# Kernel tuning notes

Measured on AMD Instinct MI355X. Metric: run time of the kernel, lower is better.

Reference implementation:

```python
import jax, jax.numpy as jnp
import numpy as np

B, N, D, R, H, E = 4, 8192, 16, 32, 64, 262144


def _linear_init(key, fan_in, fan_out):
    return jax.random.normal(key, (fan_in, fan_out), jnp.float32) * (1.0 / np.sqrt(fan_in))


def setup_inputs() -> dict:
    key = jax.random.key(0)
    ks = jax.random.split(key, 8)
    particles = jax.random.normal(ks[0], (B, N, D), jnp.float32)
    senders = jax.random.randint(ks[1], (E,), 0, N, dtype=jnp.int32)
    receivers = jax.random.randint(ks[2], (E,), 0, N, dtype=jnp.int32)
    # relation_encoder: Linear(2D->H), ReLU, Linear(H->R), ReLU
    W1 = _linear_init(ks[3], 2 * D, H)
    b1 = jnp.zeros((H,), jnp.float32)
    W2 = _linear_init(ks[4], H, R)
    b2 = jnp.zeros((R,), jnp.float32)
    # dynamics_fn: Linear(D+R->H), ReLU, Linear(H->D)
    W3 = _linear_init(ks[5], D + R, H)
    b3 = jnp.zeros((H,), jnp.float32)
    W4 = _linear_init(ks[6], H, D)
    b4 = jnp.zeros((D,), jnp.float32)
    return {"particles": particles, "senders": senders, "receivers": receivers,
            "W1": W1, "b1": b1, "W2": W2, "b2": b2,
            "W3": W3, "b3": b3, "W4": W4, "b4": b4}


def reference(particles, senders, receivers, W1, b1, W2, b2, W3, b3, W4, b4):
    # Gather per-edge sender/receiver states: [B, E, D]
    send = particles[:, senders, :]
    recv = particles[:, receivers, :]
    edge_in = jnp.concatenate([send, recv], axis=-1)          # [B, E, 2D]
    # relation_encoder (one batched GEMM over all edges)
    h = jax.nn.relu(edge_in @ W1 + b1)                        # [B, E, H]
    rel_feat = jax.nn.relu(h @ W2 + b2)                       # [B, E, R]
    # scatter-add edge features into receiver nodes
    Bp, Np, _ = particles.shape
    rel = jnp.zeros((Bp, Np, rel_feat.shape[-1]), particles.dtype)
    rel = rel.at[:, receivers, :].add(rel_feat)               # [B, N, R]
    # node update MLP
    dyn_in = jnp.concatenate([particles, rel], axis=-1)       # [B, N, D+R]
    delta = jax.nn.relu(dyn_in @ W3 + b3) @ W4 + b4           # [B, N, D]
    return particles + delta
```

## Files before the change

### kernel.cpp

```cpp
#include <hip/hip_runtime.h>
#include <hip/hip_bf16.h>

namespace {

constexpr int B = 4;
constexpr int N = 8192;
constexpr int D = 16;
constexpr int R = 32;
constexpr int H = 64;
constexpr int E = 262144;

typedef __attribute__((ext_vector_type(8))) short short8;
typedef __attribute__((ext_vector_type(4))) short short4v;
typedef __attribute__((ext_vector_type(4))) float f32x4;

__device__ __forceinline__ float4 ld4(const float* p) {
    return *reinterpret_cast<const float4*>(p);
}
__device__ __forceinline__ float4 fma4(float a, float4 w, float4 c) {
    return float4{fmaf(a, w.x, c.x), fmaf(a, w.y, c.y),
                  fmaf(a, w.z, c.z), fmaf(a, w.w, c.w)};
}
__device__ __forceinline__ float4 relu4(float4 v) {
    return float4{fmaxf(v.x, 0.f), fmaxf(v.y, 0.f), fmaxf(v.z, 0.f), fmaxf(v.w, 0.f)};
}
__device__ __forceinline__ short bf16s(float f) {
    __hip_bfloat16 h = __float2bfloat16(f);
    return __builtin_bit_cast(short, h);
}
__device__ __forceinline__ short8 pack8(float4 a, float4 b) {
    short8 o;
    o[0] = bf16s(a.x); o[1] = bf16s(a.y); o[2] = bf16s(a.z); o[3] = bf16s(a.w);
    o[4] = bf16s(b.x); o[5] = bf16s(b.y); o[6] = bf16s(b.z); o[7] = bf16s(b.w);
    return o;
}
__device__ __forceinline__ short4v pack4_relu(f32x4 c) {
    short4v o;
    o[0] = bf16s(fmaxf(c[0], 0.f)); o[1] = bf16s(fmaxf(c[1], 0.f));
    o[2] = bf16s(fmaxf(c[2], 0.f)); o[3] = bf16s(fmaxf(c[3], 0.f));
    return o;
}

constexpr int RED_S = 260;

__global__ __launch_bounds__(256) void hist_prepack_kernel(
    const int* __restrict__ receivers, int* __restrict__ cnt,
    const float* __restrict__ W1, const float* __restrict__ W2,
    const float* __restrict__ W3, const float* __restrict__ W4,
    short* __restrict__ w1p, short* __restrict__ w2p,
    short* __restrict__ w3p, short* __restrict__ w4p,
    float4* __restrict__ relz)
{
    if (blockIdx.x < 1024) {
        int e = blockIdx.x * 256 + threadIdx.x;
        atomicAdd(cnt + receivers[e], 1);
        return;
    }
    if (blockIdx.x >= 1025) {
        const int base = (blockIdx.x - 1025) * 256 + threadIdx.x;
        #pragma unroll
        for (int i = 0; i < 8; ++i)
            relz[base + i * 32768] = float4{0.f, 0.f, 0.f, 0.f};
        return;
    }
    const int t = threadIdx.x;
    for (int i = t; i < 4 * 64 * 8; i += 256) {
        int j = i & 7, lane = (i >> 3) & 63, ct = i >> 9;
        int k = (lane >> 4) * 8 + j, n = ct * 16 + (lane & 15);
        w1p[i] = bf16s(W1[k * H + n]);
    }
    for (int i = t; i < 4 * 64 * 8; i += 256) {
        int j = i & 7, lane = (i >> 3) & 63, idx = i >> 9;
        int ct = idx >> 1, kc = idx & 1;
        int k = kc * 32 + (lane >> 4) * 8 + j, f = ct * 16 + (lane & 15);
        w2p[i] = bf16s(W2[k * R + f]);
    }
    for (int i = t; i < 8 * 64 * 8; i += 256) {
        int j = i & 7, lane = (i >> 3) & 63, idx = i >> 9;
        int ct = idx >> 1, kc = idx & 1;
        int k = kc * 32 + (lane >> 4) * 8 + j, n = ct * 16 + (lane & 15);
        w3p[i] = (k < D + R) ? bf16s(W3[k * H + n]) : (short)0;
    }
    for (int i = t; i < 2 * 64 * 8; i += 256) {
        int j = i & 7, lane = (i >> 3) & 63, kc = i >> 9;
        int k = kc * 32 + (lane >> 4) * 8 + j, d = lane & 15;
        w4p[i] = bf16s(W4[k * D + d]);
    }
}

__global__ __launch_bounds__(1024) void scan_kernel(
    const int* __restrict__ cnt, int* __restrict__ pos)
{
    __shared__ int wtot[16];
    const int t = threadIdx.x;
    const int lane = t & 63;
    int local[8];
    int s = 0;
    #pragma unroll
    for (int i = 0; i < 8; ++i) { local[i] = cnt[t * 8 + i]; s += local[i]; }
    int incl = s;
    #pragma unroll
    for (int d = 1; d < 64; d <<= 1) {
        int v = __shfl_up(incl, d, 64);
        if (lane >= d) incl += v;
    }
    if (lane == 63) wtot[t >> 6] = incl;
    __syncthreads();
    int base = incl - s;
    const int wv = t >> 6;
    #pragma unroll
    for (int i = 0; i < 16; ++i) base += (i < wv) ? wtot[i] : 0;
    #pragma unroll
    for (int i = 0; i < 8; ++i) {
        pos[t * 8 + i] = base;
        base += local[i];
    }
}

__global__ __launch_bounds__(256) void scatter_kernel(
    const int* __restrict__ senders, const int* __restrict__ receivers,
    int* __restrict__ pos, int2* __restrict__ sr)
{
    int e = blockIdx.x * 256 + threadIdx.x;
    if (e < E) {
        int r = receivers[e];
        int p = atomicAdd(pos + r, 1);
        sr[p] = int2{senders[e], r};
    }
}

__global__ __launch_bounds__(256, 3) void edge_mfma_kernel(
    const float* __restrict__ particles,
    const int2*  __restrict__ sr,
    const short* __restrict__ w1p, const float* __restrict__ b1,
    const short* __restrict__ w2p, const float* __restrict__ b2,
    float* __restrict__ rel)
{
    __shared__ float red[31 * RED_S + 256];
    __shared__ short hbuf[4][16 * 72];
    __shared__ int   rs[256];

    const int tid  = threadIdx.x;
    const int lane = tid & 63;
    const int w    = tid >> 6;
    const int b    = blockIdx.x >> 10;
    const int p0   = (blockIdx.x & 1023) * 256;
    const int l15  = lane & 15;
    const int q    = lane >> 4;

    const int2 srv = sr[p0 + tid];
    const int sval = srv.x;
    const int rval = srv.y;
    rs[tid] = rval;

    float4 a0[4], a1[4];
    #pragma unroll
    for (int t = 0; t < 4; ++t) {
        int srow = __shfl(sval, t * 16 + l15);
        int rrow = __shfl(rval, t * 16 + l15);
        int row = (q < 2) ? srow : rrow;
        const float* src = particles + ((size_t)b * N + row) * D + (q & 1) * 8;
        a0[t] = ld4(src);
        a1[t] = ld4(src + 4);
    }

    short8 w1f[4], w2f[4];
    #pragma unroll
    for (int mt = 0; mt < 4; ++mt)
        w1f[mt] = *reinterpret_cast<const short8*>(w1p + (mt * 64 + lane) * 8);
    #pragma unroll
    for (int i = 0; i < 4; ++i)
        w2f[i] = *reinterpret_cast<const short8*>(w2p + (i * 64 + lane) * 8);

    f32x4 bias1[4];
    #pragma unroll
    for (int mt = 0; mt < 4; ++mt) {
        float4 t4 = ld4(b1 + mt * 16 + q * 4);
        bias1[mt] = f32x4{t4.x, t4.y, t4.z, t4.w};
    }
    const float bias2a = b2[l15];
    const float bias2b = b2[16 + l15];

    short8 af[4];
    #pragma unroll
    for (int t = 0; t < 4; ++t) af[t] = pack8(a0[t], a1[t]);

    short* hb = &hbuf[w][0];

    #pragma unroll
    for (int t = 0; t < 4; ++t) {
        #pragma unroll
        for (int mt = 0; mt < 4; ++mt) {
            f32x4 c = bias1[mt];
            c = __builtin_amdgcn_mfma_f32_16x16x32_bf16(w1f[mt], af[t], c, 0, 0, 0);
            *reinterpret_cast<short4v*>(hb + l15 * 72 + mt * 16 + q * 4) = pack4_relu(c);
        }
        short8 h0 = *reinterpret_cast<const short8*>(hb + l15 * 72 + q * 8);
        short8 h1 = *reinterpret_cast<const short8*>(hb + l15 * 72 + 32 + q * 8);

        f32x4 r0 = {bias2a, bias2a, bias2a, bias2a};
        f32x4 r1 = {bias2b, bias2b, bias2b, bias2b};
        r0 = __builtin_amdgcn_mfma_f32_16x16x32_bf16(h0, w2f[0], r0, 0, 0, 0);
        r0 = __builtin_amdgcn_mfma_f32_16x16x32_bf16(h1, w2f[1], r0, 0, 0, 0);
        r1 = __builtin_amdgcn_mfma_f32_16x16x32_bf16(h0, w2f[2], r1, 0, 0, 0);
        r1 = __builtin_amdgcn_mfma_f32_16x16x32_bf16(h1, w2f[3], r1, 0, 0, 0);

        const int pb = w * 64 + t * 16 + q * 4;
        *reinterpret_cast<f32x4*>(red + l15 * RED_S + pb) =
            f32x4{fmaxf(r0[0], 0.f), fmaxf(r0[1], 0.f), fmaxf(r0[2], 0.f), fmaxf(r0[3], 0.f)};
        *reinterpret_cast<f32x4*>(red + (16 + l15) * RED_S + pb) =
            f32x4{fmaxf(r1[0], 0.f), fmaxf(r1[1], 0.f), fmaxf(r1[2], 0.f), fmaxf(r1[3], 0.f)};
    }
    __syncthreads();

    const int g = tid >> 5;
    const int f = tid & 31;
    const int base = g * 32;

    f32x4 v4[8];
    #pragma unroll
    for (int i = 0; i < 8; ++i)
        v4[i] = *reinterpret_cast<const f32x4*>(red + f * RED_S + base + 4 * i);
    int4 r4[8];
    #pragma unroll
    for (int i = 0; i < 8; ++i)
        r4[i] = *reinterpret_cast<const int4*>(rs + base + 4 * i);

    const int first = r4[0].x;
    const int last  = r4[7].w;
    if (first == last) {
        float acc = 0.f;
        #pragma unroll
        for (int i = 0; i < 8; ++i)
            acc += (v4[i][0] + v4[i][1]) + (v4[i][2] + v4[i][3]);
        atomicAdd(rel + ((size_t)b * N + first) * R + f, acc);
    } else {
        float acc = 0.f;
        int cur = first;
        #pragma unroll
        for (int i = 0; i < 32; ++i) {
            int rr = (i & 3) == 0 ? r4[i >> 2].x : (i & 3) == 1 ? r4[i >> 2].y
                   : (i & 3) == 2 ? r4[i >> 2].z : r4[i >> 2].w;
            float v = v4[i >> 2][i & 3];
            if (rr != cur) {
                atomicAdd(rel + ((size_t)b * N + cur) * R + f, acc);
                acc = 0.f;
                cur = rr;
            }
            acc += v;
        }
        atomicAdd(rel + ((size_t)b * N + cur) * R + f, acc);
    }
}

__global__ __launch_bounds__(256, 4) void node_mfma_kernel(
    const float* __restrict__ particles,
    const float* __restrict__ rel,
    const short* __restrict__ w3p, const float* __restrict__ b3,
    const short* __restrict__ w4p, const float* __restrict__ b4,
    float* __restrict__ out)
{
    __shared__ short hbuf[4][16 * 72];

    const int tid  = threadIdx.x;
    const int lane = tid & 63;
    const int w    = tid >> 6;
    const int tile = blockIdx.x * 4 + w;
    const int b    = tile >> 9;
    const int l15  = lane & 15;
    const int q    = lane >> 4;
    const int node = (tile & 511) * 16 + l15;

    const float* prow = particles + ((size_t)b * N + node) * D;
    const float* rrow = rel + ((size_t)b * N + node) * R;

    const float* src0 = (q < 2) ? (prow + (q & 1) * 8) : (rrow + (q & 1) * 8);
    float4 c0a = ld4(src0), c0b = ld4(src0 + 4);
    float4 c1a = {0.f, 0.f, 0.f, 0.f}, c1b = {0.f, 0.f, 0.f, 0.f};
    if (q < 2) { c1a = ld4(rrow + 16 + q * 8); c1b = ld4(rrow + 20 + q * 8); }

    short8 w3f[8], w4f[2];
    #pragma unroll
    for (int i = 0; i < 8; ++i)
        w3f[i] = *reinterpret_cast<const short8*>(w3p + (i * 64 + lane) * 8);
    #pragma unroll
    for (int i = 0; i < 2; ++i)
        w4f[i] = *reinterpret_cast<const short8*>(w4p + (i * 64 + lane) * 8);

    f32x4 bias3[4];
    #pragma unroll
    for (int mt = 0; mt < 4; ++mt) {
        float4 t4 = ld4(b3 + mt * 16 + q * 4);
        bias3[mt] = f32x4{t4.x, t4.y, t4.z, t4.w};
    }
    f32x4 bias4;
    { float4 t4 = ld4(b4 + q * 4); bias4 = f32x4{t4.x, t4.y, t4.z, t4.w}; }

    short8 a0 = pack8(c0a, c0b);
    short8 a1 = pack8(c1a, c1b);

    short* hb = &hbuf[w][0];
    #pragma unroll
    for (int mt = 0; mt < 4; ++mt) {
        f32x4 c = bias3[mt];
        c = __builtin_amdgcn_mfma_f32_16x16x32_bf16(w3f[mt * 2 + 0], a0, c, 0, 0, 0);
        c = __builtin_amdgcn_mfma_f32_16x16x32_bf16(w3f[mt * 2 + 1], a1, c, 0, 0, 0);
        *reinterpret_cast<short4v*>(hb + l15 * 72 + mt * 16 + q * 4) = pack4_relu(c);
    }
    short8 h0 = *reinterpret_cast<const short8*>(hb + l15 * 72 + q * 8);
    short8 h1 = *reinterpret_cast<const short8*>(hb + l15 * 72 + 32 + q * 8);

    f32x4 r = bias4;
    r = __builtin_amdgcn_mfma_f32_16x16x32_bf16(w4f[0], h0, r, 0, 0, 0);
    r = __builtin_amdgcn_mfma_f32_16x16x32_bf16(w4f[1], h1, r, 0, 0, 0);

    float4 pv = ld4(prow + q * 4);
    float4* po = reinterpret_cast<float4*>(out + ((size_t)b * N + node) * D + q * 4);
    *po = float4{pv.x + r[0], pv.y + r[1], pv.z + r[2], pv.w + r[3]};
}


__global__ __launch_bounds__(256, 2) void edge_atomic_kernel(
    const float* __restrict__ particles,
    const int*   __restrict__ senders,
    const int*   __restrict__ receivers,
    const float* __restrict__ W1, const float* __restrict__ b1,
    const float* __restrict__ W2, const float* __restrict__ b2,
    float* __restrict__ rel)
{
    const int idx = blockIdx.x * 256 + threadIdx.x;
    const int b = idx >> 18;
    const int e = idx & (E - 1);
    const int s = senders[e];
    const int r = receivers[e];

    float4 ein4[8];
    {
        const float4* ps = reinterpret_cast<const float4*>(particles + ((size_t)b * N + s) * D);
        const float4* pr = reinterpret_cast<const float4*>(particles + ((size_t)b * N + r) * D);
        #pragma unroll
        for (int qq = 0; qq < 4; ++qq) ein4[qq] = ps[qq];
        #pragma unroll
        for (int qq = 0; qq < 4; ++qq) ein4[4 + qq] = pr[qq];
    }
    float4 rf4[8];
    #pragma unroll
    for (int qq = 0; qq < 8; ++qq) rf4[qq] = ld4(b2 + 4 * qq);

    for (int j4 = 0; j4 < H / 4; ++j4) {
        float4 h = ld4(b1 + 4 * j4);
        const float* w1c = W1 + 4 * j4;
        #pragma unroll
        for (int kv = 0; kv < 8; ++kv) {
            const float4 ev = ein4[kv];
            h = fma4(ev.x, ld4(w1c + (4 * kv + 0) * H), h);
            h = fma4(ev.y, ld4(w1c + (4 * kv + 1) * H), h);
            h = fma4(ev.z, ld4(w1c + (4 * kv + 2) * H), h);
            h = fma4(ev.w, ld4(w1c + (4 * kv + 3) * H), h);
        }
        h = relu4(h);
        const float* w2r = W2 + (4 * j4) * R;
        #pragma unroll
        for (int qq = 0; qq < 4; ++qq) {
            const float hq = (qq == 0) ? h.x : (qq == 1) ? h.y : (qq == 2) ? h.z : h.w;
            #pragma unroll
            for (int r4 = 0; r4 < 8; ++r4)
                rf4[r4] = fma4(hq, ld4(w2r + qq * R + 4 * r4), rf4[r4]);
        }
    }
    float* dst = rel + ((size_t)b * N + r) * R;
    #pragma unroll
    for (int r4 = 0; r4 < 8; ++r4) {
        float4 v = relu4(rf4[r4]);
        atomicAdd(dst + 4 * r4 + 0, v.x);
        atomicAdd(dst + 4 * r4 + 1, v.y);
        atomicAdd(dst + 4 * r4 + 2, v.z);
        atomicAdd(dst + 4 * r4 + 3, v.w);
    }
}

__global__ __launch_bounds__(256, 2) void node_valu_kernel(
    const float* __restrict__ particles,
    const float* __restrict__ rel,
    const float* __restrict__ W3, const float* __restrict__ b3,
    const float* __restrict__ W4, const float* __restrict__ b4,
    float* __restrict__ out)
{
    const int idx = blockIdx.x * 256 + threadIdx.x;
    float4 in4[12];
    {
        const float4* pp = reinterpret_cast<const float4*>(particles + (size_t)idx * D);
        #pragma unroll
        for (int qq = 0; qq < 4; ++qq) in4[qq] = pp[qq];
        const float4* pr = reinterpret_cast<const float4*>(rel + (size_t)idx * R);
        #pragma unroll
        for (int qq = 0; qq < 8; ++qq) in4[4 + qq] = pr[qq];
    }
    float4 dl4[4];
    #pragma unroll
    for (int qq = 0; qq < 4; ++qq) dl4[qq] = ld4(b4 + 4 * qq);

    for (int j4 = 0; j4 < H / 4; ++j4) {
        float4 h = ld4(b3 + 4 * j4);
        const float* w3c = W3 + 4 * j4;
        #pragma unroll
        for (int kv = 0; kv < 12; ++kv) {
            const float4 ev = in4[kv];
            h = fma4(ev.x, ld4(w3c + (4 * kv + 0) * H), h);
            h = fma4(ev.y, ld4(w3c + (4 * kv + 1) * H), h);
            h = fma4(ev.z, ld4(w3c + (4 * kv + 2) * H), h);
            h = fma4(ev.w, ld4(w3c + (4 * kv + 3) * H), h);
        }
        h = relu4(h);
        const float* w4r = W4 + (4 * j4) * D;
        #pragma unroll
        for (int qq = 0; qq < 4; ++qq) {
            const float hq = (qq == 0) ? h.x : (qq == 1) ? h.y : (qq == 2) ? h.z : h.w;
            #pragma unroll
            for (int d4 = 0; d4 < 4; ++d4)
                dl4[d4] = fma4(hq, ld4(w4r + qq * D + 4 * d4), dl4[d4]);
        }
    }
    float4* po = reinterpret_cast<float4*>(out + (size_t)idx * D);
    #pragma unroll
    for (int qq = 0; qq < 4; ++qq) {
        float4 v = dl4[qq];
        float4 pv = in4[qq];
        po[qq] = float4{pv.x + v.x, pv.y + v.y, pv.z + v.z, pv.w + v.w};
    }
}

}

extern "C" void kernel_launch(void* const* d_in, const int* in_sizes, int n_in,
                              void* d_out, int out_size, void* d_ws, size_t ws_size,
                              hipStream_t stream) {
    const float* particles = (const float*)d_in[0];
    const int*   senders   = (const int*)d_in[1];
    const int*   receivers = (const int*)d_in[2];
    const float* W1 = (const float*)d_in[3];
    const float* b1 = (const float*)d_in[4];
    const float* W2 = (const float*)d_in[5];
    const float* b2 = (const float*)d_in[6];
    const float* W3 = (const float*)d_in[7];
    const float* b3 = (const float*)d_in[8];
    const float* W4 = (const float*)d_in[9];
    const float* b4 = (const float*)d_in[10];
    float* out = (float*)d_out;

    char* ws = (char*)d_ws;
    size_t off = 0;
    auto take = [&](size_t bytes) -> char* {
        char* p = ws + off;
        off = (off + bytes + 255) & ~(size_t)255;
        return p;
    };
    int*   cnt     = (int*)  take((size_t)N * 4);
    int*   pos     = (int*)  take((size_t)N * 4);
    int2*  sr      = (int2*) take((size_t)E * 8);
    float* rel     = (float*)take((size_t)B * N * R * 4);
    short* w1p     = (short*)take((size_t)4 * 64 * 8 * 2);
    short* w2p     = (short*)take((size_t)4 * 64 * 8 * 2);
    short* w3p     = (short*)take((size_t)8 * 64 * 8 * 2);
    short* w4p     = (short*)take((size_t)2 * 64 * 8 * 2);
    const bool fast = (off <= ws_size);

    if (fast) {
        hipMemsetAsync(cnt, 0, (size_t)N * 4, stream);
        hist_prepack_kernel<<<1025 + 128, 256, 0, stream>>>(
            receivers, cnt, W1, W2, W3, W4, w1p, w2p, w3p, w4p, (float4*)rel);
        scan_kernel<<<1, 1024, 0, stream>>>(cnt, pos);
        scatter_kernel<<<E / 256, 256, 0, stream>>>(senders, receivers, pos, sr);
        edge_mfma_kernel<<<(B * E) / 256, 256, 0, stream>>>(
            particles, sr, w1p, b1, w2p, b2, rel);
        node_mfma_kernel<<<(B * N / 16) / 4, 256, 0, stream>>>(
            particles, rel, w3p, b3, w4p, b4, out);
    } else {
        float* rel0 = (float*)d_ws;
        hipMemsetAsync(rel0, 0, (size_t)B * N * R * 4, stream);
        edge_atomic_kernel<<<(B * E) / 256, 256, 0, stream>>>(
            particles, senders, receivers, W1, b1, W2, b2, rel0);
        node_valu_kernel<<<(B * N) / 256, 256, 0, stream>>>(
            particles, rel0, W3, b3, W4, b4, out);
    }
}
```

Measured before the change: 140.0 us.

## Fuse sort preprocessing into one cooperative kernel and shrink edge reduction buffer to bf16

Replaces the memset, histogram/prepack, scan and scatter launches with a single cooperative kernel that uses grid-wide syncs between phases. This removes several kernel launch gaps and the separate memset. The edge kernel also stores its per-edge relation features as bf16 in shared memory instead of fp32, which halves LDS use and allows a higher occupancy hint (4 blocks per CU). The cost is lower precision in the scatter-add inputs, plus a single 1024-thread scan run by one 256-thread block. It falls back to the old path if the cooperative launch fails.

```diff
diff --git a/kernel.cpp b/kernel.cpp
--- a/kernel.cpp
+++ b/kernel.cpp
@@ -1,5 +1,8 @@
 #include <hip/hip_runtime.h>
 #include <hip/hip_bf16.h>
+#include <hip/hip_cooperative_groups.h>
+
+namespace cg = cooperative_groups;
 
 namespace {
 
@@ -40,8 +43,121 @@
     o[2] = bf16s(fmaxf(c[2], 0.f)); o[3] = bf16s(fmaxf(c[3], 0.f));
     return o;
 }
-
-constexpr int RED_S = 260;
+__device__ __forceinline__ float red_get(const int4* uu, int i) {
+    const int wsel = i >> 1;
+    const int4 v = uu[wsel >> 2];
+    const int word = (wsel & 3) == 0 ? v.x : (wsel & 3) == 1 ? v.y
+                   : (wsel & 3) == 2 ? v.z : v.w;
+    return (i & 1) ? __builtin_bit_cast(float, word & 0xffff0000)
+                   : __builtin_bit_cast(float, (unsigned)word << 16);
+}
+
+constexpr int RED_S = 264;
+
+__device__ __forceinline__ void prepack_w12(
+    int t, const float* __restrict__ W1, const float* __restrict__ W2,
+    short* __restrict__ w1p, short* __restrict__ w2p)
+{
+    for (int i = t; i < 4 * 64 * 8; i += 256) {
+        int j = i & 7, lane = (i >> 3) & 63, ct = i >> 9;
+        int k = (lane >> 4) * 8 + j, n = ct * 16 + (lane & 15);
+        w1p[i] = bf16s(W1[k * H + n]);
+    }
+    for (int i = t; i < 4 * 64 * 8; i += 256) {
+        int j = i & 7, lane = (i >> 3) & 63, idx = i >> 9;
+        int ct = idx >> 1, kc = idx & 1;
+        int k = kc * 32 + (lane >> 4) * 8 + j, f = ct * 16 + (lane & 15);
+        w2p[i] = bf16s(W2[k * R + f]);
+    }
+}
+__device__ __forceinline__ void prepack_w34(
+    int t, const float* __restrict__ W3, const float* __restrict__ W4,
+    short* __restrict__ w3p, short* __restrict__ w4p)
+{
+    for (int i = t; i < 8 * 64 * 8; i += 256) {
+        int j = i & 7, lane = (i >> 3) & 63, idx = i >> 9;
+        int ct = idx >> 1, kc = idx & 1;
+        int k = kc * 32 + (lane >> 4) * 8 + j, n = ct * 16 + (lane & 15);
+        w3p[i] = (k < D + R) ? bf16s(W3[k * H + n]) : (short)0;
+    }
+    for (int i = t; i < 2 * 64 * 8; i += 256) {
+        int j = i & 7, lane = (i >> 3) & 63, kc = i >> 9;
+        int k = kc * 32 + (lane >> 4) * 8 + j, d = lane & 15;
+        w4p[i] = bf16s(W4[k * D + d]);
+    }
+}
+
+__global__ __launch_bounds__(256) void sort_coop_kernel(
+    const int* __restrict__ senders, const int* __restrict__ receivers,
+    const float* __restrict__ W1, const float* __restrict__ W2,
+    const float* __restrict__ W3, const float* __restrict__ W4,
+    int* __restrict__ cnt, int* __restrict__ pos, int2* __restrict__ sr,
+    short* __restrict__ w1p, short* __restrict__ w2p,
+    short* __restrict__ w3p, short* __restrict__ w4p,
+    float4* __restrict__ relz)
+{
+    cg::grid_group grid = cg::this_grid();
+    const int t = threadIdx.x;
+    const int blk = blockIdx.x;
+
+    if (blk < 128) {
+        const int base = blk * 256 + t;
+        #pragma unroll
+        for (int i = 0; i < 8; ++i)
+            relz[base + i * 32768] = float4{0.f, 0.f, 0.f, 0.f};
+    } else if (blk < 160) {
+        cnt[(blk - 128) * 256 + t] = 0;
+    } else if (blk == 160) {
+        prepack_w12(t, W1, W2, w1p, w2p);
+    } else if (blk == 161) {
+        prepack_w34(t, W3, W4, w3p, w4p);
+    }
+    grid.sync();
+
+    {
+        const int base = blk * 1024 + t;
+        #pragma unroll
+        for (int i = 0; i < 4; ++i)
+            atomicAdd(cnt + receivers[base + i * 256], 1);
+    }
+    grid.sync();
+
+    if (blk == 0) {
+        __shared__ int wtot[4];
+        int local[32];
+        int s = 0;
+        #pragma unroll
+        for (int i = 0; i < 32; ++i) { local[i] = cnt[t * 32 + i]; s += local[i]; }
+        int incl = s;
+        const int lane = t & 63;
+        #pragma unroll
+        for (int d = 1; d < 64; d <<= 1) {
+            int v = __shfl_up(incl, d, 64);
+            if (lane >= d) incl += v;
+        }
+        if (lane == 63) wtot[t >> 6] = incl;
+        __syncthreads();
+        int base = incl - s;
+        const int wv = t >> 6;
+        #pragma unroll
+        for (int i = 0; i < 4; ++i) base += (i < wv) ? wtot[i] : 0;
+        #pragma unroll
+        for (int i = 0; i < 32; ++i) { pos[t * 32 + i] = base; base += local[i]; }
+    }
+    grid.sync();
+
+    {
+        const int base = blk * 1024 + t;
+        #pragma unroll
+        for (int i = 0; i < 4; ++i) {
+            const int e = base + i * 256;
+            const int r = receivers[e];
+            const int p = atomicAdd(pos + r, 1);
+            sr[p] = int2{senders[e], r};
+        }
+    }
+}
+
 
 __global__ __launch_bounds__(256) void hist_prepack_kernel(
     const int* __restrict__ receivers, int* __restrict__ cnt,
@@ -63,29 +179,8 @@
             relz[base + i * 32768] = float4{0.f, 0.f, 0.f, 0.f};
         return;
     }
-    const int t = threadIdx.x;
-    for (int i = t; i < 4 * 64 * 8; i += 256) {
-        int j = i & 7, lane = (i >> 3) & 63, ct = i >> 9;
-        int k = (lane >> 4) * 8 + j, n = ct * 16 + (lane & 15);
-        w1p[i] = bf16s(W1[k * H + n]);
-    }
-    for (int i = t; i < 4 * 64 * 8; i += 256) {
-        int j = i & 7, lane = (i >> 3) & 63, idx = i >> 9;
-        int ct = idx >> 1, kc = idx & 1;
-        int k = kc * 32 + (lane >> 4) * 8 + j, f = ct * 16 + (lane & 15);
-        w2p[i] = bf16s(W2[k * R + f]);
-    }
-    for (int i = t; i < 8 * 64 * 8; i += 256) {
-        int j = i & 7, lane = (i >> 3) & 63, idx = i >> 9;
-        int ct = idx >> 1, kc = idx & 1;
-        int k = kc * 32 + (lane >> 4) * 8 + j, n = ct * 16 + (lane & 15);
-        w3p[i] = (k < D + R) ? bf16s(W3[k * H + n]) : (short)0;
-    }
-    for (int i = t; i < 2 * 64 * 8; i += 256) {
-        int j = i & 7, lane = (i >> 3) & 63, kc = i >> 9;
-        int k = kc * 32 + (lane >> 4) * 8 + j, d = lane & 15;
-        w4p[i] = bf16s(W4[k * D + d]);
-    }
+    prepack_w12(threadIdx.x, W1, W2, w1p, w2p);
+    prepack_w34(threadIdx.x, W3, W4, w3p, w4p);
 }
 
 __global__ __launch_bounds__(1024) void scan_kernel(
@@ -129,14 +224,14 @@
     }
 }
 
-__global__ __launch_bounds__(256, 3) void edge_mfma_kernel(
+__global__ __launch_bounds__(256, 4) void edge_mfma_kernel(
     const float* __restrict__ particles,
     const int2*  __restrict__ sr,
     const short* __restrict__ w1p, const float* __restrict__ b1,
     const short* __restrict__ w2p, const float* __restrict__ b2,
     float* __restrict__ rel)
 {
-    __shared__ float red[31 * RED_S + 256];
+    __shared__ short red[R * RED_S];
     __shared__ short hbuf[4][16 * 72];
     __shared__ int   rs[256];
 
@@ -206,10 +301,8 @@
         r1 = __builtin_amdgcn_mfma_f32_16x16x32_bf16(h1, w2f[3], r1, 0, 0, 0);
 
         const int pb = w * 64 + t * 16 + q * 4;
-        *reinterpret_cast<f32x4*>(red + l15 * RED_S + pb) =
-            f32x4{fmaxf(r0[0], 0.f), fmaxf(r0[1], 0.f), fmaxf(r0[2], 0.f), fmaxf(r0[3], 0.f)};
-        *reinterpret_cast<f32x4*>(red + (16 + l15) * RED_S + pb) =
-            f32x4{fmaxf(r1[0], 0.f), fmaxf(r1[1], 0.f), fmaxf(r1[2], 0.f), fmaxf(r1[3], 0.f)};
+        *reinterpret_cast<short4v*>(red + l15 * RED_S + pb)        = pack4_relu(r0);
+        *reinterpret_cast<short4v*>(red + (16 + l15) * RED_S + pb) = pack4_relu(r1);
     }
     __syncthreads();
 
@@ -217,10 +310,10 @@
     const int f = tid & 31;
     const int base = g * 32;
 
-    f32x4 v4[8];
-    #pragma unroll
-    for (int i = 0; i < 8; ++i)
-        v4[i] = *reinterpret_cast<const f32x4*>(red + f * RED_S + base + 4 * i);
+    int4 uu[4];
+    #pragma unroll
+    for (int i = 0; i < 4; ++i)
+        uu[i] = *reinterpret_cast<const int4*>(red + f * RED_S + base + 8 * i);
     int4 r4[8];
     #pragma unroll
     for (int i = 0; i < 8; ++i)
@@ -231,8 +324,7 @@
     if (first == last) {
         float acc = 0.f;
         #pragma unroll
-        for (int i = 0; i < 8; ++i)
-            acc += (v4[i][0] + v4[i][1]) + (v4[i][2] + v4[i][3]);
+        for (int i = 0; i < 32; ++i) acc += red_get(uu, i);
         atomicAdd(rel + ((size_t)b * N + first) * R + f, acc);
     } else {
         float acc = 0.f;
@@ -241,7 +333,7 @@
         for (int i = 0; i < 32; ++i) {
             int rr = (i & 3) == 0 ? r4[i >> 2].x : (i & 3) == 1 ? r4[i >> 2].y
                    : (i & 3) == 2 ? r4[i >> 2].z : r4[i >> 2].w;
-            float v = v4[i >> 2][i & 3];
+            float v = red_get(uu, i);
             if (rr != cur) {
                 atomicAdd(rel + ((size_t)b * N + cur) * R + f, acc);
                 acc = 0.f;
@@ -466,11 +558,23 @@
     const bool fast = (off <= ws_size);
 
     if (fast) {
-        hipMemsetAsync(cnt, 0, (size_t)N * 4, stream);
-        hist_prepack_kernel<<<1025 + 128, 256, 0, stream>>>(
-            receivers, cnt, W1, W2, W3, W4, w1p, w2p, w3p, w4p, (float4*)rel);
-        scan_kernel<<<1, 1024, 0, stream>>>(cnt, pos);
-        scatter_kernel<<<E / 256, 256, 0, stream>>>(senders, receivers, pos, sr);
+        float4* relz = (float4*)rel;
+        void* cargs[] = {
+            (void*)&senders, (void*)&receivers,
+            (void*)&W1, (void*)&W2, (void*)&W3, (void*)&W4,
+            (void*)&cnt, (void*)&pos, (void*)&sr,
+            (void*)&w1p, (void*)&w2p, (void*)&w3p, (void*)&w4p,
+            (void*)&relz
+        };
+        hipError_t ce = hipLaunchCooperativeKernel(
+            (const void*)sort_coop_kernel, dim3(256), dim3(256), cargs, 0, stream);
+        if (ce != hipSuccess) {
+            hipMemsetAsync(cnt, 0, (size_t)N * 4, stream);
+            hist_prepack_kernel<<<1153, 256, 0, stream>>>(
+                receivers, cnt, W1, W2, W3, W4, w1p, w2p, w3p, w4p, relz);
+            scan_kernel<<<1, 1024, 0, stream>>>(cnt, pos);
+            scatter_kernel<<<E / 256, 256, 0, stream>>>(senders, receivers, pos, sr);
+        }
         edge_mfma_kernel<<<(B * E) / 256, 256, 0, stream>>>(
             particles, sr, w1p, b1, w2p, b2, rel);
         node_mfma_kernel<<<(B * N / 16) / 4, 256, 0, stream>>>(
```

Measured after the change: 236.2 us. 68.8% more time.

## Loop batches inside edge kernel, prefetch next batch gathers, store reduction in bf16

Applied to the files above, without the earlier changes.

The edge kernel now processes all four batches per block, so the sender/receiver index loads and row offsets are reused across batches. The particle gathers for the next batch are issued before the current batch's MFMA work to hide their latency. The shared-memory reduction buffer switches from fp32 to bf16 to halve its LDS footprint. In exchange there are four times fewer blocks, an extra barrier per batch, and the relation features lose precision before the scatter-add.

```diff
diff --git a/kernel.cpp b/kernel.cpp
--- a/kernel.cpp
+++ b/kernel.cpp
@@ -40,8 +40,50 @@
     o[2] = bf16s(fmaxf(c[2], 0.f)); o[3] = bf16s(fmaxf(c[3], 0.f));
     return o;
 }
-
-constexpr int RED_S = 260;
+__device__ __forceinline__ float red_get(const int4* uu, int i) {
+    const int wsel = i >> 1;
+    const int4 v = uu[wsel >> 2];
+    const int word = (wsel & 3) == 0 ? v.x : (wsel & 3) == 1 ? v.y
+                   : (wsel & 3) == 2 ? v.z : v.w;
+    return (i & 1) ? __builtin_bit_cast(float, word & 0xffff0000)
+                   : __builtin_bit_cast(float, (unsigned)word << 16);
+}
+
+constexpr int RED_S = 264;
+
+__device__ __forceinline__ void prepack_w12(
+    int t, const float* __restrict__ W1, const float* __restrict__ W2,
+    short* __restrict__ w1p, short* __restrict__ w2p)
+{
+    for (int i = t; i < 4 * 64 * 8; i += 256) {
+        int j = i & 7, lane = (i >> 3) & 63, ct = i >> 9;
+        int k = (lane >> 4) * 8 + j, n = ct * 16 + (lane & 15);
+        w1p[i] = bf16s(W1[k * H + n]);
+    }
+    for (int i = t; i < 4 * 64 * 8; i += 256) {
+        int j = i & 7, lane = (i >> 3) & 63, idx = i >> 9;
+        int ct = idx >> 1, kc = idx & 1;
+        int k = kc * 32 + (lane >> 4) * 8 + j, f = ct * 16 + (lane & 15);
+        w2p[i] = bf16s(W2[k * R + f]);
+    }
+}
+__device__ __forceinline__ void prepack_w34(
+    int t, const float* __restrict__ W3, const float* __restrict__ W4,
+    short* __restrict__ w3p, short* __restrict__ w4p)
+{
+    for (int i = t; i < 8 * 64 * 8; i += 256) {
+        int j = i & 7, lane = (i >> 3) & 63, idx = i >> 9;
+        int ct = idx >> 1, kc = idx & 1;
+        int k = kc * 32 + (lane >> 4) * 8 + j, n = ct * 16 + (lane & 15);
+        w3p[i] = (k < D + R) ? bf16s(W3[k * H + n]) : (short)0;
+    }
+    for (int i = t; i < 2 * 64 * 8; i += 256) {
+        int j = i & 7, lane = (i >> 3) & 63, kc = i >> 9;
+        int k = kc * 32 + (lane >> 4) * 8 + j, d = lane & 15;
+        w4p[i] = bf16s(W4[k * D + d]);
+    }
+}
+
 
 __global__ __launch_bounds__(256) void hist_prepack_kernel(
     const int* __restrict__ receivers, int* __restrict__ cnt,
@@ -63,29 +105,8 @@
             relz[base + i * 32768] = float4{0.f, 0.f, 0.f, 0.f};
         return;
     }
-    const int t = threadIdx.x;
-    for (int i = t; i < 4 * 64 * 8; i += 256) {
-        int j = i & 7, lane = (i >> 3) & 63, ct = i >> 9;
-        int k = (lane >> 4) * 8 + j, n = ct * 16 + (lane & 15);
-        w1p[i] = bf16s(W1[k * H + n]);
-    }
-    for (int i = t; i < 4 * 64 * 8; i += 256) {
-        int j = i & 7, lane = (i >> 3) & 63, idx = i >> 9;
-        int ct = idx >> 1, kc = idx & 1;
-        int k = kc * 32 + (lane >> 4) * 8 + j, f = ct * 16 + (lane & 15);
-        w2p[i] = bf16s(W2[k * R + f]);
-    }
-    for (int i = t; i < 8 * 64 * 8; i += 256) {
-        int j = i & 7, lane = (i >> 3) & 63, idx = i >> 9;
-        int ct = idx >> 1, kc = idx & 1;
-        int k = kc * 32 + (lane >> 4) * 8 + j, n = ct * 16 + (lane & 15);
-        w3p[i] = (k < D + R) ? bf16s(W3[k * H + n]) : (short)0;
-    }
-    for (int i = t; i < 2 * 64 * 8; i += 256) {
-        int j = i & 7, lane = (i >> 3) & 63, kc = i >> 9;
-        int k = kc * 32 + (lane >> 4) * 8 + j, d = lane & 15;
-        w4p[i] = bf16s(W4[k * D + d]);
-    }
+    prepack_w12(threadIdx.x, W1, W2, w1p, w2p);
+    prepack_w34(threadIdx.x, W3, W4, w3p, w4p);
 }
 
 __global__ __launch_bounds__(1024) void scan_kernel(
@@ -136,32 +157,26 @@
     const short* __restrict__ w2p, const float* __restrict__ b2,
     float* __restrict__ rel)
 {
-    __shared__ float red[31 * RED_S + 256];
+    __shared__ short red[R * RED_S];
     __shared__ short hbuf[4][16 * 72];
     __shared__ int   rs[256];
 
     const int tid  = threadIdx.x;
     const int lane = tid & 63;
     const int w    = tid >> 6;
-    const int b    = blockIdx.x >> 10;
-    const int p0   = (blockIdx.x & 1023) * 256;
+    const int p0   = blockIdx.x * 256;
     const int l15  = lane & 15;
     const int q    = lane >> 4;
 
     const int2 srv = sr[p0 + tid];
-    const int sval = srv.x;
-    const int rval = srv.y;
-    rs[tid] = rval;
-
-    float4 a0[4], a1[4];
+    rs[tid] = srv.y;
+
+    int rowoff[4];
     #pragma unroll
     for (int t = 0; t < 4; ++t) {
-        int srow = __shfl(sval, t * 16 + l15);
-        int rrow = __shfl(rval, t * 16 + l15);
-        int row = (q < 2) ? srow : rrow;
-        const float* src = particles + ((size_t)b * N + row) * D + (q & 1) * 8;
-        a0[t] = ld4(src);
-        a1[t] = ld4(src + 4);
+        int srow = __shfl(srv.x, t * 16 + l15);
+        int rrow = __shfl(srv.y, t * 16 + l15);
+        rowoff[t] = ((q < 2) ? srow : rrow) * D + (q & 1) * 8;
     }
 
     short8 w1f[4], w2f[4];
@@ -181,75 +196,96 @@
     const float bias2a = b2[l15];
     const float bias2b = b2[16 + l15];
 
-    short8 af[4];
-    #pragma unroll
-    for (int t = 0; t < 4; ++t) af[t] = pack8(a0[t], a1[t]);
+    float4 ga[4], gb[4];
+    #pragma unroll
+    for (int t = 0; t < 4; ++t) {
+        const float* src = particles + rowoff[t];
+        ga[t] = ld4(src);
+        gb[t] = ld4(src + 4);
+    }
 
     short* hb = &hbuf[w][0];
 
-    #pragma unroll
-    for (int t = 0; t < 4; ++t) {
-        #pragma unroll
-        for (int mt = 0; mt < 4; ++mt) {
-            f32x4 c = bias1[mt];
-            c = __builtin_amdgcn_mfma_f32_16x16x32_bf16(w1f[mt], af[t], c, 0, 0, 0);
-            *reinterpret_cast<short4v*>(hb + l15 * 72 + mt * 16 + q * 4) = pack4_relu(c);
-        }
-        short8 h0 = *reinterpret_cast<const short8*>(hb + l15 * 72 + q * 8);
-        short8 h1 = *reinterpret_cast<const short8*>(hb + l15 * 72 + 32 + q * 8);
-
-        f32x4 r0 = {bias2a, bias2a, bias2a, bias2a};
-        f32x4 r1 = {bias2b, bias2b, bias2b, bias2b};
-        r0 = __builtin_amdgcn_mfma_f32_16x16x32_bf16(h0, w2f[0], r0, 0, 0, 0);
-        r0 = __builtin_amdgcn_mfma_f32_16x16x32_bf16(h1, w2f[1], r0, 0, 0, 0);
-        r1 = __builtin_amdgcn_mfma_f32_16x16x32_bf16(h0, w2f[2], r1, 0, 0, 0);
-        r1 = __builtin_amdgcn_mfma_f32_16x16x32_bf16(h1, w2f[3], r1, 0, 0, 0);
-
-        const int pb = w * 64 + t * 16 + q * 4;
-        *reinterpret_cast<f32x4*>(red + l15 * RED_S + pb) =
-            f32x4{fmaxf(r0[0], 0.f), fmaxf(r0[1], 0.f), fmaxf(r0[2], 0.f), fmaxf(r0[3], 0.f)};
-        *reinterpret_cast<f32x4*>(red + (16 + l15) * RED_S + pb) =
-            f32x4{fmaxf(r1[0], 0.f), fmaxf(r1[1], 0.f), fmaxf(r1[2], 0.f), fmaxf(r1[3], 0.f)};
-    }
-    __syncthreads();
-
-    const int g = tid >> 5;
-    const int f = tid & 31;
-    const int base = g * 32;
-
-    f32x4 v4[8];
-    #pragma unroll
-    for (int i = 0; i < 8; ++i)
-        v4[i] = *reinterpret_cast<const f32x4*>(red + f * RED_S + base + 4 * i);
-    int4 r4[8];
-    #pragma unroll
-    for (int i = 0; i < 8; ++i)
-        r4[i] = *reinterpret_cast<const int4*>(rs + base + 4 * i);
-
-    const int first = r4[0].x;
-    const int last  = r4[7].w;
-    if (first == last) {
-        float acc = 0.f;
-        #pragma unroll
-        for (int i = 0; i < 8; ++i)
-            acc += (v4[i][0] + v4[i][1]) + (v4[i][2] + v4[i][3]);
-        atomicAdd(rel + ((size_t)b * N + first) * R + f, acc);
-    } else {
-        float acc = 0.f;
-        int cur = first;
-        #pragma unroll
-        for (int i = 0; i < 32; ++i) {
-            int rr = (i & 3) == 0 ? r4[i >> 2].x : (i & 3) == 1 ? r4[i >> 2].y
-                   : (i & 3) == 2 ? r4[i >> 2].z : r4[i >> 2].w;
-            float v = v4[i >> 2][i & 3];
-            if (rr != cur) {
-                atomicAdd(rel + ((size_t)b * N + cur) * R + f, acc);
-                acc = 0.f;
-                cur = rr;
+    for (int bb = 0; bb < B; ++bb) {
+        short8 af[4];
+        #pragma unroll
+        for (int t = 0; t < 4; ++t) af[t] = pack8(ga[t], gb[t]);
+
+        if (bb + 1 < B) {
+            const float* pb = particles + (size_t)(bb + 1) * N * D;
+            #pragma unroll
+            for (int t = 0; t < 4; ++t) {
+                const float* src = pb + rowoff[t];
+                ga[t] = ld4(src);
+                gb[t] = ld4(src + 4);
             }
-            acc += v;
-        }
-        atomicAdd(rel + ((size_t)b * N + cur) * R + f, acc);
+        }
+
+        #pragma unroll
+        for (int t = 0; t < 4; ++t) {
+            #pragma unroll
+            for (int mt = 0; mt < 4; ++mt) {
+                f32x4 c = bias1[mt];
+                c = __builtin_amdgcn_mfma_f32_16x16x32_bf16(w1f[mt], af[t], c, 0, 0, 0);
+                *reinterpret_cast<short4v*>(hb + l15 * 72 + mt * 16 + q * 4) = pack4_relu(c);
+            }
+            short8 h0 = *reinterpret_cast<const short8*>(hb + l15 * 72 + q * 8);
+            short8 h1 = *reinterpret_cast<const short8*>(hb + l15 * 72 + 32 + q * 8);
+
+            f32x4 r0 = {bias2a, bias2a, bias2a, bias2a};
+            f32x4 r1 = {bias2b, bias2b, bias2b, bias2b};
+            r0 = __builtin_amdgcn_mfma_f32_16x16x32_bf16(h0, w2f[0], r0, 0, 0, 0);
+            r0 = __builtin_amdgcn_mfma_f32_16x16x32_bf16(h1, w2f[1], r0, 0, 0, 0);
+            r1 = __builtin_amdgcn_mfma_f32_16x16x32_bf16(h0, w2f[2], r1, 0, 0, 0);
+            r1 = __builtin_amdgcn_mfma_f32_16x16x32_bf16(h1, w2f[3], r1, 0, 0, 0);
+
+            const int pb2 = w * 64 + t * 16 + q * 4;
+            *reinterpret_cast<short4v*>(red + l15 * RED_S + pb2)        = pack4_relu(r0);
+            *reinterpret_cast<short4v*>(red + (16 + l15) * RED_S + pb2) = pack4_relu(r1);
+        }
+        __syncthreads();
+
+        {
+            const int g = tid >> 5;
+            const int f = tid & 31;
+            const int base = g * 32;
+            float* relb = rel + (size_t)bb * N * R;
+
+            int4 uu[4];
+            #pragma unroll
+            for (int i = 0; i < 4; ++i)
+                uu[i] = *reinterpret_cast<const int4*>(red + f * RED_S + base + 8 * i);
+            int4 r4[8];
+            #pragma unroll
+            for (int i = 0; i < 8; ++i)
+                r4[i] = *reinterpret_cast<const int4*>(rs + base + 4 * i);
+
+            const int first = r4[0].x;
+            const int last  = r4[7].w;
+            if (first == last) {
+                float acc = 0.f;
+                #pragma unroll
+                for (int i = 0; i < 32; ++i) acc += red_get(uu, i);
+                atomicAdd(relb + (size_t)first * R + f, acc);
+            } else {
+                float acc = 0.f;
+                int cur = first;
+                #pragma unroll
+                for (int i = 0; i < 32; ++i) {
+                    int rr = (i & 3) == 0 ? r4[i >> 2].x : (i & 3) == 1 ? r4[i >> 2].y
+                           : (i & 3) == 2 ? r4[i >> 2].z : r4[i >> 2].w;
+                    float v = red_get(uu, i);
+                    if (rr != cur) {
+                        atomicAdd(relb + (size_t)cur * R + f, acc);
+                        acc = 0.f;
+                        cur = rr;
+                    }
+                    acc += v;
+                }
+                atomicAdd(relb + (size_t)cur * R + f, acc);
+            }
+        }
+        __syncthreads();
     }
 }
 
@@ -467,11 +503,11 @@
 
     if (fast) {
         hipMemsetAsync(cnt, 0, (size_t)N * 4, stream);
-        hist_prepack_kernel<<<1025 + 128, 256, 0, stream>>>(
+        hist_prepack_kernel<<<1153, 256, 0, stream>>>(
             receivers, cnt, W1, W2, W3, W4, w1p, w2p, w3p, w4p, (float4*)rel);
         scan_kernel<<<1, 1024, 0, stream>>>(cnt, pos);
         scatter_kernel<<<E / 256, 256, 0, stream>>>(senders, receivers, pos, sr);
-        edge_mfma_kernel<<<(B * E) / 256, 256, 0, stream>>>(
+        edge_mfma_kernel<<<E / 256, 256, 0, stream>>>(
             particles, sr, w1p, b1, w2p, b2, rel);
         node_mfma_kernel<<<(B * N / 16) / 4, 256, 0, stream>>>(
             particles, rel, w3p, b3, w4p, b4, out);
```

After: 141.8 us. Within noise of the previous version (+1.3%).
